# Kernel optimization log

Hardware: AMD Instinct MI355X
Metric: run time of the kernel (lower is better)

## Reference

```python
import jax, jax.numpy as jnp
import numpy as np

B, T, C = 64, 256, 384
H, D = 6, 64  # num_heads, head_size

def setup_inputs() -> dict:
    key = jax.random.key(0)
    ks = jax.random.split(key, 6)
    s = 0.02
    return {
        "x": jax.random.normal(ks[0], (B, T, C), dtype=jnp.float32),
        "Wq": jax.random.normal(ks[1], (H, C, D), dtype=jnp.float32) * s,
        "Wk": jax.random.normal(ks[2], (H, C, D), dtype=jnp.float32) * s,
        "Wv": jax.random.normal(ks[3], (H, C, D), dtype=jnp.float32) * s,
        "Wp": jax.random.normal(ks[4], (C, C), dtype=jnp.float32) * s,
        "bp": jnp.zeros((C,), dtype=jnp.float32),
    }

def reference(x, Wq, Wk, Wv, Wp, bp):
    # per-head projections: [B,T,C] x [H,C,D] -> [B,H,T,D]
    q = jnp.einsum('btc,hcd->bhtd', x, Wq)
    k = jnp.einsum('btc,hcd->bhtd', x, Wk)
    v = jnp.einsum('btc,hcd->bhtd', x, Wv)
    scale = 1.0 / jnp.sqrt(jnp.float32(D))
    scores = jnp.einsum('bhtd,bhsd->bhts', q, k) * scale  # [B,H,T,T]
    Tlen = x.shape[1]
    causal = jnp.tril(jnp.ones((Tlen, Tlen), dtype=bool))
    scores = jnp.where(causal, scores, -jnp.inf)
    wei = jax.nn.softmax(scores, axis=-1)
    # dropout is identity in eval mode
    out = jnp.einsum('bhts,bhsd->bhtd', wei, v)  # [B,H,T,D]
    # concat heads in order (matches torch.cat over head list)
    out = jnp.transpose(out, (0, 2, 1, 3)).reshape(x.shape[0], Tlen, H * D)
    return out @ Wp.T + bp  # nn.Linear: y = x W^T + b
```

## Files before the change

kernel.cpp:

```cpp
#include <hip/hip_runtime.h>

constexpr int Bn = 64, T = 256, C = 384, H = 6, D = 64;
constexpr int BT = Bn * T;
constexpr int NQKV = 3 * C;
constexpr int WALL_ELEMS = NQKV * C;
constexpr int WP_ELEMS = C * C;

using f32x4 = __attribute__((ext_vector_type(4))) float;
using fvec4 = __attribute__((ext_vector_type(4))) float;
using us4   = __attribute__((ext_vector_type(4))) unsigned short;
using us8   = __attribute__((ext_vector_type(8))) unsigned short;
using bf8   = __attribute__((ext_vector_type(8))) __bf16;

__device__ __forceinline__ unsigned short f2bf(float f) {
  unsigned u = __builtin_bit_cast(unsigned, f);
  u += 0x7FFFu + ((u >> 16) & 1u);
  return (unsigned short)(u >> 16);
}

__device__ __forceinline__ f32x4 mfma16(us8 a, us8 b, f32x4 c) {
  return __builtin_amdgcn_mfma_f32_16x16x32_bf16(
      __builtin_bit_cast(bf8, a), __builtin_bit_cast(bf8, b), c, 0, 0, 0);
}

__device__ __forceinline__ void glds16(const unsigned short* g,
                                       unsigned short* l) {
  __builtin_amdgcn_global_load_lds(
      (const __attribute__((address_space(1))) unsigned int*)g,
      (__attribute__((address_space(3))) unsigned int*)l, 16, 0, 0);
}

__global__ __launch_bounds__(256) void k_prep(
    const float* __restrict__ x,
    const float* __restrict__ Wq, const float* __restrict__ Wk,
    const float* __restrict__ Wv, const float* __restrict__ Wp,
    unsigned short* __restrict__ Wall, unsigned short* __restrict__ Wpb,
    unsigned short* __restrict__ Xb) {
  __shared__ unsigned short t[64][71];
  const int bid = blockIdx.x;
  const int tid = threadIdx.x;
  if (bid < 108) {
    const int ct = bid % 6, ph = bid / 6;
    const int h = ph % 6, p = ph / 6;
    const float* W = (p == 0) ? Wq : (p == 1) ? Wk : Wv;
    const int c0 = ct * 64;
    const int d = tid & 63, cq = tid >> 6;
#pragma unroll
    for (int s = 0; s < 16; ++s) {
      const int c_loc = cq * 16 + s;
      t[c_loc][d] = f2bf(W[(size_t)(h * C + c0 + c_loc) * D + d]);
    }
    __syncthreads();
    const int d_loc = tid >> 2, ch = tid & 3;
#pragma unroll
    for (int it = 0; it < 2; ++it) {
      const int cc = (ch + it * 4) * 8;
      us8 o;
#pragma unroll
      for (int j = 0; j < 8; ++j) o[j] = t[cc + j][d_loc];
      *(us8*)&Wall[(size_t)(p * C + h * D + d_loc) * C + c0 + cc] = o;
    }
  } else {
    const float* src;
    unsigned short* dst;
    int off;
    if (bid < 180) { src = Wp; dst = Wpb; off = (bid - 108) * 2048 + tid * 8; }
    else           { src = x;  dst = Xb;  off = (bid - 180) * 2048 + tid * 8; }
    fvec4 a = *(const fvec4*)(src + off);
    fvec4 b = *(const fvec4*)(src + off + 4);
    us8 o;
#pragma unroll
    for (int j = 0; j < 4; ++j) { o[j] = f2bf(a[j]); o[4 + j] = f2bf(b[j]); }
    *(us8*)(dst + off) = o;
  }
}

__device__ __forceinline__ void stage_tile(
    const unsigned short* __restrict__ g, unsigned short* l,
    int row0g, int k0, int tr, int tc, int w) {
#pragma unroll
  for (int s = 0; s < 4; ++s) {
    const int row = s * 32 + tr;
    const int sc = (tc ^ (row & 7)) * 8;
    glds16(g + (size_t)(row0g + row) * C + k0 + sc,
           l + (s * 32 + w * 8) * 64);
  }
}

template <int MODE>
__global__ __launch_bounds__(256) void k_gemm(
    const unsigned short* __restrict__ A, const unsigned short* __restrict__ Bm,
    const float* __restrict__ bias, unsigned short* __restrict__ QKV,
    unsigned short* __restrict__ VT, float* __restrict__ Of, int nwgn) {
  constexpr int BK = 64, NT = C / BK;
  __shared__ unsigned short Al[2][128 * BK];
  __shared__ unsigned short Bl[2][128 * BK];
  const int nwg = gridDim.x;
  const int bid = blockIdx.x;
  const int lin = (bid & 7) * (nwg >> 3) + (bid >> 3);
  const int m0 = (lin / nwgn) * 128, n0 = (lin % nwgn) * 128;
  const int tid = threadIdx.x;
  const int w = tid >> 6, lane = tid & 63;
  const int lr = lane & 15, lg = lane >> 4;
  const int wm = (w >> 1) * 64, wn = (w & 1) * 64;
  const int tr = tid >> 3, tc = tid & 7;

  f32x4 acc[4][4];
#pragma unroll
  for (int i = 0; i < 4; ++i)
#pragma unroll
    for (int j = 0; j < 4; ++j) acc[i][j] = (f32x4){0.f, 0.f, 0.f, 0.f};

  stage_tile(A, &Al[0][0], m0, 0, tr, tc, w);
  stage_tile(Bm, &Bl[0][0], n0, 0, tr, tc, w);
  stage_tile(A, &Al[1][0], m0, BK, tr, tc, w);
  stage_tile(Bm, &Bl[1][0], n0, BK, tr, tc, w);

  int cur = 0;
  for (int t = 0; t < NT; ++t) {
    if (t < NT - 1) {
      asm volatile("s_waitcnt vmcnt(8)" ::: "memory");
    } else {
      asm volatile("s_waitcnt vmcnt(0)" ::: "memory");
    }
    asm volatile("s_barrier" ::: "memory");
#pragma unroll
    for (int kc = 0; kc < 2; ++kc) {
      us8 af[4], bfr[4];
#pragma unroll
      for (int i = 0; i < 4; ++i) {
        const int ra = wm + i * 16 + lr;
        af[i] = *(const us8*)&Al[cur][ra * 64 + (((kc * 4 + lg) ^ (ra & 7)) * 8)];
        const int rb = wn + i * 16 + lr;
        bfr[i] = *(const us8*)&Bl[cur][rb * 64 + (((kc * 4 + lg) ^ (rb & 7)) * 8)];
      }
#pragma unroll
      for (int i = 0; i < 4; ++i)
#pragma unroll
        for (int j = 0; j < 4; ++j)
          acc[i][j] = mfma16(af[i], bfr[j], acc[i][j]);
    }
    asm volatile("s_barrier" ::: "memory");
    if (t + 2 < NT) {
      stage_tile(A, &Al[cur][0], m0, (t + 2) * BK, tr, tc, w);
      stage_tile(Bm, &Bl[cur][0], n0, (t + 2) * BK, tr, tc, w);
    }
    cur ^= 1;
  }

  if (MODE == 1) {
#pragma unroll
    for (int i = 0; i < 4; ++i)
#pragma unroll
      for (int j = 0; j < 4; ++j) {
        const int col = n0 + wn + j * 16 + lr;
        const float bv = bias[col];
#pragma unroll
        for (int r = 0; r < 4; ++r) {
          const size_t row = m0 + wm + i * 16 + lg * 4 + r;
          Of[row * C + col] = acc[i][j][r] + bv;
        }
      }
  } else if (n0 < 2 * C) {
    const float scl = (n0 < C) ? 0.18033688f : 1.0f;
#pragma unroll
    for (int i = 0; i < 4; ++i)
#pragma unroll
      for (int j = 0; j < 4; ++j) {
        const int col = n0 + wn + j * 16 + lr;
#pragma unroll
        for (int r = 0; r < 4; ++r) {
          const size_t row = m0 + wm + i * 16 + lg * 4 + r;
          QKV[row * NQKV + col] = f2bf(acc[i][j][r] * scl);
        }
      }
  } else {
#pragma unroll
    for (int i = 0; i < 4; ++i)
#pragma unroll
      for (int j = 0; j < 4; ++j) {
        const int vcol = n0 + wn + j * 16 + lr - 2 * C;
        const int h = vcol >> 6, d = vcol & 63;
        const int row0 = m0 + wm + i * 16 + lg * 4;
        const int b = row0 >> 8, tq = row0 & 255;
        us4 o4;
#pragma unroll
        for (int r = 0; r < 4; ++r) o4[r] = f2bf(acc[i][j][r]);
        *(us4*)&VT[(((size_t)b * H + h) * D + d) * T + tq] = o4;
      }
  }
}

__global__ __launch_bounds__(512, 4) void k_attn(
    const unsigned short* __restrict__ QKV, const unsigned short* __restrict__ VT,
    unsigned short* __restrict__ Y) {
  __shared__ unsigned short Kl[2][128][64];
  __shared__ unsigned short Vl[2][64][128];
  __shared__ unsigned short Pch[8][16][32];
  const int bid = blockIdx.x;
  const int lin = (bid & 7) * 96 + (bid >> 3);
  const int b = lin / 12, rr = lin % 12;
  const int h = rr >> 1, qt = rr & 1;
  const int t0 = qt * 128;
  const int nt = qt + 1;
  const int tid = threadIdx.x;
  const int w = tid >> 6, lane = tid & 63;
  const int lr = lane & 15, lg = lane >> 4;
  const int xk = lr & 7;

  const size_t qbase = (size_t)(b * T + t0 + w * 16 + lr) * NQKV + h * D;
  const us8 aq0 = *(const us8*)(QKV + qbase + lg * 8);
  const us8 aq1 = *(const us8*)(QKV + qbase + 32 + lg * 8);
  asm volatile("" ::: "memory");

  const unsigned short* kgbase = QKV + (size_t)(b * T) * NQKV + C + h * D;
  const unsigned short* vbase = VT + ((size_t)b * H + h) * D * T;

  auto stage_kv = [&](int tt) {
#pragma unroll
    for (int s = 0; s < 2; ++s) {
      const int row = s * 64 + w * 8 + (lane >> 3);
      glds16(kgbase + (size_t)(tt * 128 + row) * NQKV + ((lane & 7) ^ (row & 7)) * 8,
             &Kl[tt][s * 64 + w * 8][0]);
    }
#pragma unroll
    for (int s = 0; s < 2; ++s) {
      const int d = s * 32 + w * 4 + (lane >> 4);
      glds16(vbase + (size_t)d * T + tt * 128 + (((lane & 15) ^ (d & 7)) * 8),
             &Vl[tt][s * 32 + w * 4][0]);
    }
  };

  stage_kv(0);
  if (nt == 2) stage_kv(1);

  if (nt == 2) asm volatile("s_waitcnt vmcnt(4)" ::: "memory");
  else         asm volatile("s_waitcnt vmcnt(0)" ::: "memory");
  asm volatile("s_barrier" ::: "memory");

  float m[4], l[4];
  f32x4 o[4];
#pragma unroll
  for (int nf = 0; nf < 4; ++nf) o[nf] = (f32x4){0.f, 0.f, 0.f, 0.f};

  auto process_tile = [&](int tt, bool need_mask, bool first) {
    f32x4 s[8];
#pragma unroll
    for (int sf = 0; sf < 8; ++sf) s[sf] = (f32x4){0.f, 0.f, 0.f, 0.f};
#pragma unroll
    for (int sf = 0; sf < 8; ++sf) {
      us8 kb0 = *(const us8*)&Kl[tt][sf * 16 + lr][(lg ^ xk) * 8];
      s[sf] = mfma16(aq0, kb0, s[sf]);
      us8 kb1 = *(const us8*)&Kl[tt][sf * 16 + lr][((4 + lg) ^ xk) * 8];
      s[sf] = mfma16(aq1, kb1, s[sf]);
    }
    float tm[4] = {-1e30f, -1e30f, -1e30f, -1e30f};
#pragma unroll
    for (int sf = 0; sf < 8; ++sf) {
#pragma unroll
      for (int r = 0; r < 4; ++r) {
        float v = s[sf][r];
        if (need_mask) {
          const int trow = t0 + w * 16 + lg * 4 + r;
          const int scol = tt * 128 + sf * 16 + lr;
          if (scol > trow) v = -1e30f;
          s[sf][r] = v;
        }
        tm[r] = fmaxf(tm[r], v);
      }
    }
#pragma unroll
    for (int dd = 1; dd < 16; dd <<= 1)
#pragma unroll
      for (int r = 0; r < 4; ++r)
        tm[r] = fmaxf(tm[r], __shfl_xor(tm[r], dd, 64));
    float fac[4];
    if (first) {
#pragma unroll
      for (int r = 0; r < 4; ++r) m[r] = tm[r];
    } else {
#pragma unroll
      for (int r = 0; r < 4; ++r) {
        const float mn = fmaxf(m[r], tm[r]);
        fac[r] = __builtin_amdgcn_exp2f(m[r] - mn);
        m[r] = mn;
      }
    }
    float ts[4] = {0.f, 0.f, 0.f, 0.f};
#pragma unroll
    for (int sf = 0; sf < 8; ++sf) {
#pragma unroll
      for (int r = 0; r < 4; ++r) {
        float p = __builtin_amdgcn_exp2f(s[sf][r] - m[r]);
        s[sf][r] = p;
        ts[r] += p;
      }
    }
#pragma unroll
    for (int dd = 1; dd < 16; dd <<= 1)
#pragma unroll
      for (int r = 0; r < 4; ++r)
        ts[r] += __shfl_xor(ts[r], dd, 64);
    if (first) {
#pragma unroll
      for (int r = 0; r < 4; ++r) l[r] = ts[r];
    } else {
#pragma unroll
      for (int r = 0; r < 4; ++r) l[r] = l[r] * fac[r] + ts[r];
#pragma unroll
      for (int nf = 0; nf < 4; ++nf)
#pragma unroll
        for (int r = 0; r < 4; ++r) o[nf][r] *= fac[r];
    }
#pragma unroll
    for (int kk = 0; kk < 4; ++kk) {
#pragma unroll
      for (int half = 0; half < 2; ++half) {
        const int sf = kk * 2 + half;
        const int row = lg * 4;
#pragma unroll
        for (int r = 0; r < 4; ++r) {
          const int cch = (half * 2 + (lr >> 3)) ^ ((row + r) & 3);
          Pch[w][row + r][cch * 8 + (lr & 7)] = f2bf(s[sf][r]);
        }
      }
      __builtin_amdgcn_wave_barrier();
      us8 pa = *(const us8*)&Pch[w][lr][(lg ^ (lr & 3)) * 8];
      __builtin_amdgcn_wave_barrier();
#pragma unroll
      for (int nf = 0; nf < 4; ++nf) {
        us8 bv = *(const us8*)&Vl[tt][nf * 16 + lr][((kk * 4 + lg) ^ xk) * 8];
        o[nf] = mfma16(pa, bv, o[nf]);
      }
    }
  };

  process_tile(0, qt == 0, true);
  if (nt == 2) {
    asm volatile("s_waitcnt vmcnt(0)" ::: "memory");
    asm volatile("s_barrier" ::: "memory");
    process_tile(1, true, false);
  }

  float rs[4];
#pragma unroll
  for (int r = 0; r < 4; ++r) rs[r] = 1.0f / l[r];
#pragma unroll
  for (int nf = 0; nf < 4; ++nf)
#pragma unroll
    for (int r = 0; r < 4; ++r) {
      const int trow = t0 + w * 16 + lg * 4 + r;
      Y[(size_t)(b * T + trow) * C + h * D + nf * 16 + lr] =
          f2bf(o[nf][r] * rs[r]);
    }
}

extern "C" void kernel_launch(void* const* d_in, const int* in_sizes, int n_in,
                              void* d_out, int out_size, void* d_ws, size_t ws_size,
                              hipStream_t stream) {
  const float* x  = (const float*)d_in[0];
  const float* Wq = (const float*)d_in[1];
  const float* Wk = (const float*)d_in[2];
  const float* Wv = (const float*)d_in[3];
  const float* Wp = (const float*)d_in[4];
  const float* bp = (const float*)d_in[5];
  float* out = (float*)d_out;

  unsigned short* Wall = (unsigned short*)d_ws;
  unsigned short* Wpb  = Wall + WALL_ELEMS;
  unsigned short* QKV  = Wpb + WP_ELEMS;
  unsigned short* Yb   = QKV + (size_t)BT * NQKV;
  unsigned short* VT   = Yb + (size_t)BT * C;
  unsigned short* Xb   = Yb;

  k_prep<<<180 + BT * C / 2048, 256, 0, stream>>>(x, Wq, Wk, Wv, Wp,
                                                  Wall, Wpb, Xb);
  k_gemm<0><<<NQKV / 128 * (BT / 128), 256, 0, stream>>>(
      Xb, Wall, nullptr, QKV, VT, nullptr, NQKV / 128);
  k_attn<<<T / 128 * H * Bn, 512, 0, stream>>>(QKV, VT, Yb);
  k_gemm<1><<<C / 128 * (BT / 128), 256, 0, stream>>>(
      Yb, Wpb, bp, nullptr, nullptr, out, C / 128);
}
```

Baseline: 67.06 us.

## Fuse fp32-to-bf16 conversion of x into the QKV GEMM A-tile load

Drops the separate pass that converts x to bf16 in the prep kernel. The QKV GEMM now loads fp32 x tiles straight into LDS and converts them to bf16 in registers with v_cvt_pk_bf16_f32 before each MFMA. This avoids writing and re-reading a bf16 copy of x. In exchange, the A tile becomes single-buffered fp32, which doubles its LDS traffic, and the per-fragment conversion adds ALU work and a second barrier-bounded stage inside the k-loop.

New measurement: 71.98 us. +7.3%, slower.

```diff
diff --git a/kernel.cpp b/kernel.cpp
--- a/kernel.cpp
+++ b/kernel.cpp
@@ -8,6 +8,7 @@
 
 using f32x4 = __attribute__((ext_vector_type(4))) float;
 using fvec4 = __attribute__((ext_vector_type(4))) float;
+using u32x4 = __attribute__((ext_vector_type(4))) unsigned int;
 using us4   = __attribute__((ext_vector_type(4))) unsigned short;
 using us8   = __attribute__((ext_vector_type(8))) unsigned short;
 using bf8   = __attribute__((ext_vector_type(8))) __bf16;
@@ -23,19 +24,16 @@
       __builtin_bit_cast(bf8, a), __builtin_bit_cast(bf8, b), c, 0, 0, 0);
 }
 
-__device__ __forceinline__ void glds16(const unsigned short* g,
-                                       unsigned short* l) {
+__device__ __forceinline__ void glds16(const void* g, void* l) {
   __builtin_amdgcn_global_load_lds(
       (const __attribute__((address_space(1))) unsigned int*)g,
       (__attribute__((address_space(3))) unsigned int*)l, 16, 0, 0);
 }
 
 __global__ __launch_bounds__(256) void k_prep(
-    const float* __restrict__ x,
     const float* __restrict__ Wq, const float* __restrict__ Wk,
     const float* __restrict__ Wv, const float* __restrict__ Wp,
-    unsigned short* __restrict__ Wall, unsigned short* __restrict__ Wpb,
-    unsigned short* __restrict__ Xb) {
+    unsigned short* __restrict__ Wall, unsigned short* __restrict__ Wpb) {
   __shared__ unsigned short t[64][71];
   const int bid = blockIdx.x;
   const int tid = threadIdx.x;
@@ -61,17 +59,13 @@
       *(us8*)&Wall[(size_t)(p * C + h * D + d_loc) * C + c0 + cc] = o;
     }
   } else {
-    const float* src;
-    unsigned short* dst;
-    int off;
-    if (bid < 180) { src = Wp; dst = Wpb; off = (bid - 108) * 2048 + tid * 8; }
-    else           { src = x;  dst = Xb;  off = (bid - 180) * 2048 + tid * 8; }
-    fvec4 a = *(const fvec4*)(src + off);
-    fvec4 b = *(const fvec4*)(src + off + 4);
+    const int off = (bid - 108) * 2048 + tid * 8;
+    fvec4 a = *(const fvec4*)(Wp + off);
+    fvec4 b = *(const fvec4*)(Wp + off + 4);
     us8 o;
 #pragma unroll
     for (int j = 0; j < 4; ++j) { o[j] = f2bf(a[j]); o[4 + j] = f2bf(b[j]); }
-    *(us8*)(dst + off) = o;
+    *(us8*)(Wpb + off) = o;
   }
 }
 
@@ -87,18 +81,119 @@
   }
 }
 
-template <int MODE>
-__global__ __launch_bounds__(256) void k_gemm(
+__global__ __launch_bounds__(256) void k_gemm0(
+    const float* __restrict__ X, const unsigned short* __restrict__ Bm,
+    unsigned short* __restrict__ QKV, unsigned short* __restrict__ VT) {
+  constexpr int BK = 64, NT = C / BK;
+  __shared__ float Af[128 * BK];
+  __shared__ unsigned short Bl[2][128 * BK];
+  const int nwg = gridDim.x;
+  const int bid = blockIdx.x;
+  const int lin = (bid & 7) * (nwg >> 3) + (bid >> 3);
+  const int m0 = (lin / 9) * 128, n0 = (lin % 9) * 128;
+  const int tid = threadIdx.x;
+  const int w = tid >> 6, lane = tid & 63;
+  const int lr = lane & 15, lg = lane >> 4;
+  const int wm = (w >> 1) * 64, wn = (w & 1) * 64;
+  const int tr = tid >> 3, tc = tid & 7;
+
+  auto stageA = [&](int k0) {
+#pragma unroll
+    for (int s = 0; s < 8; ++s) {
+      const int row = w * 32 + s * 4 + (lane >> 4);
+      const int sc = (lane & 15) ^ ((row & 7) << 1);
+      glds16(X + (size_t)(m0 + row) * C + k0 + sc * 4,
+             Af + (w * 32 + s * 4) * 64);
+    }
+  };
+
+  f32x4 acc[4][4];
+#pragma unroll
+  for (int i = 0; i < 4; ++i)
+#pragma unroll
+    for (int j = 0; j < 4; ++j) acc[i][j] = (f32x4){0.f, 0.f, 0.f, 0.f};
+
+  stage_tile(Bm, &Bl[0][0], n0, 0, tr, tc, w);
+  stageA(0);
+  int curB = 0;
+  for (int t = 0; t < NT; ++t) {
+    if (t + 1 < NT) {
+      stage_tile(Bm, &Bl[curB ^ 1][0], n0, (t + 1) * BK, tr, tc, w);
+      asm volatile("s_waitcnt vmcnt(4)" ::: "memory");
+    } else {
+      asm volatile("s_waitcnt vmcnt(0)" ::: "memory");
+    }
+    asm volatile("s_barrier" ::: "memory");
+#pragma unroll
+    for (int kc = 0; kc < 2; ++kc) {
+      us8 af[4], bfr[4];
+#pragma unroll
+      for (int i = 0; i < 4; ++i) {
+        const int ra = wm + i * 16 + lr;
+        const int c0 = (kc * 4 + lg) * 2;
+        const int off = ra * 64 + ((c0 ^ ((ra & 7) << 1)) * 4);
+        fvec4 lo = *(const fvec4*)&Af[off];
+        fvec4 hi = *(const fvec4*)&Af[off + 4];
+        unsigned p0, p1, p2, p3;
+        asm("v_cvt_pk_bf16_f32 %0, %1, %2" : "=v"(p0) : "v"(lo[0]), "v"(lo[1]));
+        asm("v_cvt_pk_bf16_f32 %0, %1, %2" : "=v"(p1) : "v"(lo[2]), "v"(lo[3]));
+        asm("v_cvt_pk_bf16_f32 %0, %1, %2" : "=v"(p2) : "v"(hi[0]), "v"(hi[1]));
+        asm("v_cvt_pk_bf16_f32 %0, %1, %2" : "=v"(p3) : "v"(hi[2]), "v"(hi[3]));
+        af[i] = __builtin_bit_cast(us8, (u32x4){p0, p1, p2, p3});
+        const int rb = wn + i * 16 + lr;
+        bfr[i] = *(const us8*)&Bl[curB][rb * 64 + (((kc * 4 + lg) ^ (rb & 7)) * 8)];
+      }
+#pragma unroll
+      for (int i = 0; i < 4; ++i)
+#pragma unroll
+        for (int j = 0; j < 4; ++j)
+          acc[i][j] = mfma16(af[i], bfr[j], acc[i][j]);
+    }
+    asm volatile("s_barrier" ::: "memory");
+    if (t + 1 < NT) stageA((t + 1) * BK);
+    curB ^= 1;
+  }
+
+  if (n0 < 2 * C) {
+    const float scl = (n0 < C) ? 0.18033688f : 1.0f;
+#pragma unroll
+    for (int i = 0; i < 4; ++i)
+#pragma unroll
+      for (int j = 0; j < 4; ++j) {
+        const int col = n0 + wn + j * 16 + lr;
+#pragma unroll
+        for (int r = 0; r < 4; ++r) {
+          const size_t row = m0 + wm + i * 16 + lg * 4 + r;
+          QKV[row * NQKV + col] = f2bf(acc[i][j][r] * scl);
+        }
+      }
+  } else {
+#pragma unroll
+    for (int i = 0; i < 4; ++i)
+#pragma unroll
+      for (int j = 0; j < 4; ++j) {
+        const int vcol = n0 + wn + j * 16 + lr - 2 * C;
+        const int h = vcol >> 6, d = vcol & 63;
+        const int row0 = m0 + wm + i * 16 + lg * 4;
+        const int b = row0 >> 8, tq = row0 & 255;
+        us4 o4;
+#pragma unroll
+        for (int r = 0; r < 4; ++r) o4[r] = f2bf(acc[i][j][r]);
+        *(us4*)&VT[(((size_t)b * H + h) * D + d) * T + tq] = o4;
+      }
+  }
+}
+
+__global__ __launch_bounds__(256) void k_gemm1(
     const unsigned short* __restrict__ A, const unsigned short* __restrict__ Bm,
-    const float* __restrict__ bias, unsigned short* __restrict__ QKV,
-    unsigned short* __restrict__ VT, float* __restrict__ Of, int nwgn) {
+    const float* __restrict__ bias, float* __restrict__ Of) {
   constexpr int BK = 64, NT = C / BK;
   __shared__ unsigned short Al[2][128 * BK];
   __shared__ unsigned short Bl[2][128 * BK];
   const int nwg = gridDim.x;
   const int bid = blockIdx.x;
   const int lin = (bid & 7) * (nwg >> 3) + (bid >> 3);
-  const int m0 = (lin / nwgn) * 128, n0 = (lin % nwgn) * 128;
+  const int m0 = (lin / 3) * 128, n0 = (lin % 3) * 128;
   const int tid = threadIdx.x;
   const int w = tid >> 6, lane = tid & 63;
   const int lr = lane & 15, lg = lane >> 4;
@@ -148,47 +243,18 @@
     cur ^= 1;
   }
 
-  if (MODE == 1) {
-#pragma unroll
-    for (int i = 0; i < 4; ++i)
-#pragma unroll
-      for (int j = 0; j < 4; ++j) {
-        const int col = n0 + wn + j * 16 + lr;
-        const float bv = bias[col];
-#pragma unroll
-        for (int r = 0; r < 4; ++r) {
-          const size_t row = m0 + wm + i * 16 + lg * 4 + r;
-          Of[row * C + col] = acc[i][j][r] + bv;
-        }
-      }
-  } else if (n0 < 2 * C) {
-    const float scl = (n0 < C) ? 0.18033688f : 1.0f;
-#pragma unroll
-    for (int i = 0; i < 4; ++i)
-#pragma unroll
-      for (int j = 0; j < 4; ++j) {
-        const int col = n0 + wn + j * 16 + lr;
-#pragma unroll
-        for (int r = 0; r < 4; ++r) {
-          const size_t row = m0 + wm + i * 16 + lg * 4 + r;
-          QKV[row * NQKV + col] = f2bf(acc[i][j][r] * scl);
-        }
-      }
-  } else {
-#pragma unroll
-    for (int i = 0; i < 4; ++i)
-#pragma unroll
-      for (int j = 0; j < 4; ++j) {
-        const int vcol = n0 + wn + j * 16 + lr - 2 * C;
-        const int h = vcol >> 6, d = vcol & 63;
-        const int row0 = m0 + wm + i * 16 + lg * 4;
-        const int b = row0 >> 8, tq = row0 & 255;
-        us4 o4;
-#pragma unroll
-        for (int r = 0; r < 4; ++r) o4[r] = f2bf(acc[i][j][r]);
-        *(us4*)&VT[(((size_t)b * H + h) * D + d) * T + tq] = o4;
-      }
-  }
+#pragma unroll
+  for (int i = 0; i < 4; ++i)
+#pragma unroll
+    for (int j = 0; j < 4; ++j) {
+      const int col = n0 + wn + j * 16 + lr;
+      const float bv = bias[col];
+#pragma unroll
+      for (int r = 0; r < 4; ++r) {
+        const size_t row = m0 + wm + i * 16 + lg * 4 + r;
+        Of[row * C + col] = acc[i][j][r] + bv;
+      }
+    }
 }
 
 __global__ __launch_bounds__(512, 4) void k_attn(
@@ -371,13 +437,9 @@
   unsigned short* QKV  = Wpb + WP_ELEMS;
   unsigned short* Yb   = QKV + (size_t)BT * NQKV;
   unsigned short* VT   = Yb + (size_t)BT * C;
-  unsigned short* Xb   = Yb;
-
-  k_prep<<<180 + BT * C / 2048, 256, 0, stream>>>(x, Wq, Wk, Wv, Wp,
-                                                  Wall, Wpb, Xb);
-  k_gemm<0><<<NQKV / 128 * (BT / 128), 256, 0, stream>>>(
-      Xb, Wall, nullptr, QKV, VT, nullptr, NQKV / 128);
+
+  k_prep<<<180, 256, 0, stream>>>(Wq, Wk, Wv, Wp, Wall, Wpb);
+  k_gemm0<<<NQKV / 128 * (BT / 128), 256, 0, stream>>>(x, Wall, QKV, VT);
   k_attn<<<T / 128 * H * Bn, 512, 0, stream>>>(QKV, VT, Yb);
-  k_gemm<1><<<C / 128 * (BT / 128), 256, 0, stream>>>(
-      Yb, Wpb, bp, nullptr, nullptr, out, C / 128);
-}
+  k_gemm1<<<C / 128 * (BT / 128), 256, 0, stream>>>(Yb, Wpb, bp, out);
+}
```
